# Kernel tuning notes

Hardware: AMD Instinct MI355X
Metric: run time of the kernel (lower is better)

## Reference

```python
import jax, jax.numpy as jnp
import numpy as np
from jax import lax

SLOPE = 0.01  # nn.LeakyReLU default negative slope

def leaky(x):
    return jnp.where(x >= 0, x, SLOPE * x)

def conv2d(x, w, b, pad):
    # x: [N,C,H,W], w: [O,I,kh,kw]
    y = lax.conv_general_dilated(x, w, (1, 1), [(pad, pad), (pad, pad)],
                                 dimension_numbers=('NCHW', 'OIHW', 'NCHW'))
    return y + b[None, :, None, None]

def centered_ifftn(x, axes):
    # np.fft.fftshift(np.fft.ifftn(np.fft.ifftshift(X), norm='ortho'))
    return jnp.fft.fftshift(jnp.fft.ifftn(jnp.fft.ifftshift(x, axes=axes), axes=axes, norm='ortho'), axes=axes)

def setup_inputs() -> dict:
    key = jax.random.key(0)
    ks = jax.random.split(key, 10)
    B, H, W, CK = 8, 640, 368, 32
    return {
        'img':    jax.random.normal(ks[0], (B, 1, H, W), jnp.float32),
        'kspace': jax.random.normal(ks[1], (B, 2, H, W), jnp.float32),
        # k_model1: Conv2d(2, CK, 3, padding=1) + LeakyReLU
        'wk': jax.random.normal(ks[2], (CK, 2, 3, 3), jnp.float32) * 0.1,
        'bk': jnp.zeros((CK,), jnp.float32),
        # conv1: Conv2d(CK, 2, kernel_size=1)
        'w1': jax.random.normal(ks[3], (2, CK, 1, 1), jnp.float32) * 0.1,
        'b1': jnp.zeros((2,), jnp.float32),
        # conv2: Conv2d(2, 1, kernel_size=1)
        'w2': jax.random.normal(ks[4], (1, 2, 1, 1), jnp.float32) * 0.1,
        'b2': jnp.zeros((1,), jnp.float32),
        # i_model1: Conv2d(1, 1, 3, padding=1) + LeakyReLU
        'wi': jax.random.normal(ks[5], (1, 1, 3, 3), jnp.float32) * 0.1,
        'bi': jnp.zeros((1,), jnp.float32),
    }

def reference(img, kspace, wk, bk, w1, b1, w2, b2, wi, bi):
    # k-space branch: k_model1 then conv1 + LeakyReLU
    out1 = leaky(conv2d(leaky(conv2d(kspace, wk, bk, 1)), w1, b1, 0))  # [B,2,H,W]
    # channel 0 = real, channel 1 = imag; ifftn over ALL axes (incl. batch),
    # exactly as the original numpy call with axes=range(out.ndim)
    cplx = out1[:, 0].astype(jnp.complex64) + 1j * out1[:, 1].astype(jnp.complex64)  # [B,H,W]
    im = jnp.abs(centered_ifftn(cplx, (0, 1, 2)))[:, None]  # [B,1,H,W]
    # concat with image, cast to half (torch.cuda.HalfTensor), conv2 + LeakyReLU
    out = jnp.concatenate([im, img], axis=1).astype(jnp.float16)  # [B,2,H,W]
    out = leaky(conv2d(out, w2.astype(jnp.float16), b2.astype(jnp.float16), 0))
    out = out.astype(jnp.float32)  # [B,1,H,W]
    # image-domain model
    return leaky(conv2d(out, wi, bi, 1))  # [B,1,H,W]
```

## Files before the change

### kernel.cpp

```cpp
#include <hip/hip_runtime.h>
#include <hip/hip_fp16.h>
#include <math.h>

#define B_ 8
#define H_ 640
#define W_ 368
#define HW_ (H_*W_)
#define NP_ (B_*H_*W_)

#define WLINES 8
#define HLINES 4
#define HP 645
#define TS 16

typedef __attribute__((ext_vector_type(8))) short v8s;
typedef __attribute__((ext_vector_type(4))) float v4f;

__device__ __forceinline__ float leaky_(float x){ return fmaxf(x, 0.01f*x); }

__device__ __forceinline__ unsigned short f2bf(float x){
    unsigned u = __float_as_uint(x);
    u += 0x7FFFu + ((u >> 16) & 1u);
    return (unsigned short)(u >> 16);
}

__device__ __forceinline__ float2 cadd_(float2 a, float2 b){ return make_float2(a.x+b.x, a.y+b.y); }
__device__ __forceinline__ float2 csub_(float2 a, float2 b){ return make_float2(a.x-b.x, a.y-b.y); }
__device__ __forceinline__ float2 cmul_(float2 a, float c, float s){
    return make_float2(a.x*c - a.y*s, a.x*s + a.y*c);
}
__device__ __forceinline__ float2 cmulv_(float2 a, float2 w){
    return make_float2(a.x*w.x - a.y*w.y, a.x*w.y + a.y*w.x);
}

__device__ __forceinline__ void dft4p_(float2 p0, float2 p1, float2 p2, float2 p3,
                                       float2& z0, float2& z1, float2& z2, float2& z3){
    float2 s0 = cadd_(p0,p2), d0 = csub_(p0,p2);
    float2 s1 = cadd_(p1,p3), d1 = csub_(p1,p3);
    z0 = cadd_(s0,s1);
    z2 = csub_(s0,s1);
    z1 = make_float2(d0.x - d1.y, d0.y + d1.x);
    z3 = make_float2(d0.x + d1.y, d0.y - d1.x);
}

__device__ __forceinline__ void fft16p_(const float2* x, float2* X){
    const float C1 = 0.9238795325112867f, S1 = 0.3826834323650898f;
    const float R  = 0.7071067811865476f;
    float2 Y[4][4];
    #pragma unroll
    for (int b = 0; b < 4; ++b)
        dft4p_(x[b], x[4+b], x[8+b], x[12+b], Y[b][0], Y[b][1], Y[b][2], Y[b][3]);
    Y[1][1] = cmul_(Y[1][1],  C1,  S1);
    Y[1][2] = cmul_(Y[1][2],   R,   R);
    Y[1][3] = cmul_(Y[1][3],  S1,  C1);
    Y[2][1] = cmul_(Y[2][1],   R,   R);
    Y[2][2] = make_float2(-Y[2][2].y, Y[2][2].x);
    Y[2][3] = cmul_(Y[2][3],  -R,   R);
    Y[3][1] = cmul_(Y[3][1],  S1,  C1);
    Y[3][2] = cmul_(Y[3][2],  -R,   R);
    Y[3][3] = cmul_(Y[3][3], -C1, -S1);
    #pragma unroll
    for (int c = 0; c < 4; ++c)
        dft4p_(Y[0][c], Y[1][c], Y[2][c], Y[3][c], X[c], X[c+4], X[c+8], X[c+12]);
}

__device__ __forceinline__ void fft8p_(const float2* x, float2* X){
    const float R = 0.7071067811865476f;
    float2 Y0[4], Y1[4];
    dft4p_(x[0], x[2], x[4], x[6], Y0[0], Y0[1], Y0[2], Y0[3]);
    dft4p_(x[1], x[3], x[5], x[7], Y1[0], Y1[1], Y1[2], Y1[3]);
    float2 T0 = Y1[0];
    float2 T1 = cmul_(Y1[1],  R, R);
    float2 T2 = make_float2(-Y1[2].y, Y1[2].x);
    float2 T3 = cmul_(Y1[3], -R, R);
    X[0] = cadd_(Y0[0], T0);  X[4] = csub_(Y0[0], T0);
    X[1] = cadd_(Y0[1], T1);  X[5] = csub_(Y0[1], T1);
    X[2] = cadd_(Y0[2], T2);  X[6] = csub_(Y0[2], T2);
    X[3] = cadd_(Y0[3], T3);  X[7] = csub_(Y0[3], T3);
}

__global__ void init_tables_kernel(float2* __restrict__ T){
    int i = blockIdx.x*blockDim.x + threadIdx.x;
    if (i >= 1301) return;
    int r, c, modN; int j;
    if      (i <  368){ j = i;        r = j%16; c = j/16; modN = 368; }
    else if (i < 1008){ j = i-368;    r = j%16; c = j/16; modN = 640; }
    else if (i < 1048){ j = i-1008;   r = j%8;  c = j/8;  modN = 40;  }
    else              { j = i-1048;   r = j/11; c = j%11 + 1; modN = 23; }
    int t = (int)(((long long)r * c) % modN);
    if (t > modN/2) t -= modN;
    float ang = (float)(6.283185307179586 * ((double)t / (double)modN));
    float s, co;
    sincosf(ang, &s, &co);
    T[i] = make_float2(co, s);
}

__global__ __launch_bounds__(256) void kbranch_mfma(const float* __restrict__ ksp,
                               const float* __restrict__ wk,
                               const float* __restrict__ bk,
                               const float* __restrict__ w1,
                               const float* __restrict__ b1,
                               float2* __restrict__ A){
    __shared__ unsigned short Sb[2616];
    __shared__ unsigned short Wr[4*512];
    int t = threadIdx.x;
    int bh = blockIdx.x;
    int h = bh % 640, b = bh / 640;

    for (int i = t; i < 2616; i += 256){
        float val = 0.f;
        if (i < 2232){
            int rr = i / 372, col = i - rr*372;
            int r = rr >> 1, ic = rr & 1;
            int hh = h - 1 + r, sc = col - 1;
            if ((unsigned)hh < 640u && (unsigned)sc < 368u)
                val = ksp[((b*2 + ic)*640 + hh)*368 + sc];
        }
        Sb[i] = f2bf(val);
    }

    int lane = t & 63, wave = t >> 6;
    int oc = lane & 15, q = lane >> 4;
    int off[8];
    v8s bf0, bf1, b2f;
    #pragma unroll
    for (int j = 0; j < 8; ++j){
        int kk = q*8 + j;
        if (kk < 18){
            int ic = (kk >= 9) ? 1 : 0;
            int tt = kk - ic*9;
            int ty = tt/3, tx = tt - ty*3;
            off[j] = (ty*2 + ic)*372 + tx;
            bf0[j] = (short)f2bf(wk[oc*18 + kk]);
            bf1[j] = (short)f2bf(wk[(oc+16)*18 + kk]);
        } else {
            off[j] = 2232;
            bf0[j] = 0; bf1[j] = 0;
        }
        b2f[j] = (oc < 2) ? (short)f2bf(w1[oc*32 + kk]) : (short)0;
    }
    float bk0 = bk[oc], bk1 = bk[oc+16];
    float biasn = (oc == 1) ? b1[1] : b1[0];
    unsigned short* Wrw = Wr + (wave << 9);
    __syncthreads();

    int gbase = wave*6;
    int cnt = (wave < 3) ? 6 : 5;
    for (int i = 0; i < cnt; ++i){
        int g = gbase + i;
        int w0m = g*16 + oc;
        v8s af;
        #pragma unroll
        for (int j = 0; j < 8; ++j) af[j] = (short)Sb[off[j] + w0m];
        v4f d0 = {0.f,0.f,0.f,0.f}, d1 = {0.f,0.f,0.f,0.f};
        d0 = __builtin_amdgcn_mfma_f32_16x16x32_bf16(af, bf0, d0, 0, 0, 0);
        d1 = __builtin_amdgcn_mfma_f32_16x16x32_bf16(af, bf1, d1, 0, 0, 0);
        #pragma unroll
        for (int r = 0; r < 4; ++r){
            int px = q*4 + r;
            Wrw[px*32 + oc]      = f2bf(leaky_(d0[r] + bk0));
            Wrw[px*32 + 16 + oc] = f2bf(leaky_(d1[r] + bk1));
        }
        asm volatile("s_waitcnt lgkmcnt(0)" ::: "memory");
        const v8s* ap = (const v8s*)(Wrw + oc*32);
        v8s a2 = ap[q];
        v4f d2 = {0.f,0.f,0.f,0.f};
        d2 = __builtin_amdgcn_mfma_f32_16x16x32_bf16(a2, b2f, d2, 0, 0, 0);
        float vals[4], ov[4];
        #pragma unroll
        for (int r = 0; r < 4; ++r){
            vals[r] = leaky_(biasn + d2[r]);
            ov[r] = __shfl_xor(vals[r], 1);
        }
        if (oc == 0){
            float2* dst = A + (size_t)bh*368 + g*16 + q*4;
            *(float4*)dst       = make_float4(vals[0], ov[0], vals[1], ov[1]);
            *(float4*)(dst + 2) = make_float4(vals[2], ov[2], vals[3], ov[3]);
        }
        asm volatile("s_waitcnt lgkmcnt(0)" ::: "memory");
    }
}

__global__ __launch_bounds__(256) void fftW_kernel(const float2* __restrict__ A,
                                                   const float2* __restrict__ TW368P,
                                                   const float2* __restrict__ F23P,
                                                   float2* __restrict__ Bt){
    __shared__ float2 X[WLINES*369];
    int t = threadIdx.x;
    size_t base = (size_t)blockIdx.x * (WLINES*368);

    for (int i = t; i < WLINES*368; i += 256){
        int l = i / 368, n = i - l*368;
        float2 v = A[base + i];
        float s = (n & 1) ? -1.f : 1.f;
        X[l*369 + n] = make_float2(v.x*s, v.y*s);
    }
    __syncthreads();

    if (t < 184){
        int l = t & 7, n2 = t >> 3;
        float2 xr[16], Xo[16];
        #pragma unroll
        for (int n1 = 0; n1 < 16; ++n1) xr[n1] = X[l*369 + 23*n1 + n2];
        fft16p_(xr, Xo);
        const float2* row = TW368P + n2*16;
        #pragma unroll
        for (int k1 = 0; k1 < 16; ++k1)
            X[l*369 + 23*k1 + n2] = cmulv_(Xo[k1], row[k1]);
    }
    __syncthreads();

    {
        int l = t & 7, k1 = (t >> 3) & 15, half = t >> 7;
        const float2* xp = X + l*369 + 23*k1;
        float2 x0 = xp[0];
        float2 u[11], d[11];
        #pragma unroll
        for (int m = 1; m <= 11; ++m){
            float2 a = xp[m], bb = xp[23-m];
            u[m-1] = cadd_(a, bb);
            d[m-1] = csub_(a, bb);
        }
        __syncthreads();
        int k2beg = half ? 12 : 0;
        int k2end = half ? 23 : 12;
        for (int k2 = k2beg; k2 < k2end; ++k2){
            const float2* row = F23P + k2*11;
            float re = x0.x, im = x0.y;
            #pragma unroll
            for (int m = 0; m < 11; ++m){
                float c = row[m].x, s = row[m].y;
                re += u[m].x*c - d[m].y*s;
                im += u[m].y*c + d[m].x*s;
            }
            X[l*369 + k1 + 16*k2] = make_float2(re, im);
        }
    }
    __syncthreads();

    const float sc = 0.052129458158616354f;
    int b  = blockIdx.x / 80;
    int h0 = (blockIdx.x - b*80) * WLINES;
    for (int i = t; i < WLINES*368; i += 256){
        int k = i >> 3, l = i & 7;
        float2 v = X[l*369 + k];
        float s = (k & 1) ? -sc : sc;
        Bt[((size_t)(b*368 + k))*640 + h0 + l] = make_float2(v.x*s, v.y*s);
    }
}

__global__ __launch_bounds__(256) void fftH_kernel(const float2* __restrict__ Bt,
                                                   const float2* __restrict__ TW640P,
                                                   const float2* __restrict__ TW40P,
                                                   float2* __restrict__ A2){
    __shared__ float2 X[HLINES*HP];
    int t = threadIdx.x;
    size_t base = (size_t)blockIdx.x * (HLINES*640);

    for (int i = t; i < HLINES*640; i += 256){
        int l = i / 640, n = i - l*640;
        float2 v = Bt[base + i];
        float s = (n & 1) ? -1.f : 1.f;
        X[l*HP + n] = make_float2(v.x*s, v.y*s);
    }
    __syncthreads();

    if (t < 160){
        int l = t & 3, n2 = t >> 2;
        float2 xr[16], Xo[16];
        #pragma unroll
        for (int n1 = 0; n1 < 16; ++n1) xr[n1] = X[l*HP + 40*n1 + n2];
        fft16p_(xr, Xo);
        const float2* row = TW640P + n2*16;
        #pragma unroll
        for (int k1 = 0; k1 < 16; ++k1)
            X[l*HP + 40*k1 + n2] = cmulv_(Xo[k1], row[k1]);
    }
    __syncthreads();

    for (int it = t; it < 320; it += 256){
        int l = it & 3, k1 = (it >> 2) & 15, m2 = it >> 6;
        float2 xr[8], Xo[8];
        #pragma unroll
        for (int m1 = 0; m1 < 8; ++m1) xr[m1] = X[l*HP + 40*k1 + 5*m1 + m2];
        fft8p_(xr, Xo);
        const float2* row = TW40P + m2*8;
        #pragma unroll
        for (int j1 = 0; j1 < 8; ++j1)
            X[l*HP + 40*k1 + 5*j1 + m2] = cmulv_(Xo[j1], row[j1]);
    }
    __syncthreads();

    {
        const float CK1[5] = {1.f,  0.30901699437494745f, -0.8090169943749475f, -0.8090169943749475f,  0.30901699437494745f};
        const float SK1[5] = {0.f,  0.9510565162951535f,   0.5877852522924731f, -0.5877852522924731f, -0.9510565162951535f};
        const float CK2[5] = {1.f, -0.8090169943749475f,   0.30901699437494745f, 0.30901699437494745f, -0.8090169943749475f};
        const float SK2[5] = {0.f,  0.5877852522924731f,  -0.9510565162951535f,  0.9510565162951535f, -0.5877852522924731f};
        int it0 = t, it1 = t + 256;
        int l0 = it0 & 3, k10 = (it0 >> 2) & 15, j10 = it0 >> 6;
        int l1 = it1 & 3, k11 = (it1 >> 2) & 15, j11 = it1 >> 6;
        float2 p0[5], p1[5];
        #pragma unroll
        for (int m2 = 0; m2 < 5; ++m2) p0[m2] = X[l0*HP + 40*k10 + 5*j10 + m2];
        #pragma unroll
        for (int m2 = 0; m2 < 5; ++m2) p1[m2] = X[l1*HP + 40*k11 + 5*j11 + m2];
        __syncthreads();
        float2 u0a = cadd_(p0[1], p0[4]), d0a = csub_(p0[1], p0[4]);
        float2 u0b = cadd_(p0[2], p0[3]), d0b = csub_(p0[2], p0[3]);
        float2 u1a = cadd_(p1[1], p1[4]), d1a = csub_(p1[1], p1[4]);
        float2 u1b = cadd_(p1[2], p1[3]), d1b = csub_(p1[2], p1[3]);
        #pragma unroll
        for (int j2 = 0; j2 < 5; ++j2){
            float c1v = CK1[j2], s1v = SK1[j2], c2v = CK2[j2], s2v = SK2[j2];
            float re0 = p0[0].x + u0a.x*c1v - d0a.y*s1v + u0b.x*c2v - d0b.y*s2v;
            float im0 = p0[0].y + u0a.y*c1v + d0a.x*s1v + u0b.y*c2v + d0b.x*s2v;
            float re1 = p1[0].x + u1a.x*c1v - d1a.y*s1v + u1b.x*c2v - d1b.y*s2v;
            float im1 = p1[0].y + u1a.y*c1v + d1a.x*s1v + u1b.y*c2v + d1b.x*s2v;
            X[l0*HP + k10 + 16*j10 + 128*j2] = make_float2(re0, im0);
            X[l1*HP + k11 + 16*j11 + 128*j2] = make_float2(re1, im1);
        }
    }
    __syncthreads();

    const float sc = 0.03952847075210474f;
    for (int i = t; i < HLINES*640; i += 256){
        int l = i / 640, k = i - l*640;
        float2 v = X[l*HP + k];
        float s = (k & 1) ? -sc : sc;
        A2[base + i] = make_float2(v.x*s, v.y*s);
    }
}

__global__ __launch_bounds__(256) void tail_kernel(const float2* __restrict__ A2,
                                  const float* __restrict__ img,
                                  const float* __restrict__ w2,
                                  const float* __restrict__ b2,
                                  const float* __restrict__ wi,
                                  const float* __restrict__ bi,
                                  float* __restrict__ out){
    __shared__ float Pl[8][TS+2][TS+3];
    int t = threadIdx.x;
    int ty0 = (blockIdx.x / 23) * TS;
    int tx0 = (blockIdx.x % 23) * TS;

    float w2h0 = __half2float(__float2half(w2[0]));
    float w2h1 = __half2float(__float2half(w2[1]));
    float b2h  = __half2float(__float2half(b2[0]));
    const float sc8 = 0.35355339059327373f;

    for (int idx = t; idx < (TS+2)*(TS+2); idx += 256){
        int hx = idx / (TS+2), hy = idx - hx*(TS+2);
        int hh = ty0 - 1 + hy, ww = tx0 - 1 + hx;
        int hc = min(max(hh, 0), H_-1), wc = min(max(ww, 0), W_-1);
        float2 x[8], Xo[8];
        #pragma unroll
        for (int n = 0; n < 8; ++n){
            float2 v = A2[((size_t)(n*368 + wc))*640 + hc];
            float s = (n & 1) ? -1.f : 1.f;
            x[n] = make_float2(v.x*s, v.y*s);
        }
        fft8p_(x, Xo);
        #pragma unroll
        for (int k = 0; k < 8; ++k){
            float s = (k & 1) ? -sc8 : sc8;
            float yr = Xo[k].x * s, yi = Xo[k].y * s;
            float mag = sqrtf(yr*yr + yi*yi);
            Pl[k][hy][hx] = __half2float(__float2half(mag));
        }
    }
    __syncthreads();

    for (int idx = t; idx < (TS+2)*(TS+2); idx += 256){
        int hy = idx / (TS+2), hx = idx - hy*(TS+2);
        int hh = ty0 - 1 + hy, ww = tx0 - 1 + hx;
        bool inb = (hh >= 0) && (hh < H_) && (ww >= 0) && (ww < W_);
        int hc = min(max(hh, 0), H_-1), wc = min(max(ww, 0), W_-1);
        float inbf = inb ? 1.f : 0.f;
        #pragma unroll
        for (int k = 0; k < 8; ++k){
            float g = __half2float(__float2half(img[(size_t)k*HW_ + hc*W_ + wc]));
            float a = Pl[k][hy][hx];
            float o = leaky_(a*w2h0 + g*w2h1 + b2h);
            o = __half2float(__float2half(o));
            Pl[k][hy][hx] = o * inbf;
        }
    }
    __syncthreads();

    int sy = t >> 4, sx = t & 15;
    float wv[9];
    #pragma unroll
    for (int q = 0; q < 9; ++q) wv[q] = wi[q];
    float bi0 = bi[0];
    #pragma unroll
    for (int k = 0; k < 8; ++k){
        float acc = bi0;
        #pragma unroll
        for (int dy = 0; dy < 3; ++dy)
            #pragma unroll
            for (int dx = 0; dx < 3; ++dx)
                acc += wv[dy*3+dx] * Pl[k][sy+dy][sx+dx];
        out[((size_t)k*H_ + ty0+sy)*W_ + tx0+sx] = leaky_(acc);
    }
}

extern "C" void kernel_launch(void* const* d_in, const int* in_sizes, int n_in,
                              void* d_out, int out_size, void* d_ws, size_t ws_size,
                              hipStream_t stream){
    const float* img = (const float*)d_in[0];
    const float* ksp = (const float*)d_in[1];
    const float* wk  = (const float*)d_in[2];
    const float* bk  = (const float*)d_in[3];
    const float* w1  = (const float*)d_in[4];
    const float* b1  = (const float*)d_in[5];
    const float* w2  = (const float*)d_in[6];
    const float* b2  = (const float*)d_in[7];
    const float* wi  = (const float*)d_in[8];
    const float* bi  = (const float*)d_in[9];

    char* ws = (char*)d_ws;
    float2* A   = (float2*)(ws + 0);
    float2* Bt  = (float2*)(ws + 15073280);
    float2* T   = (float2*)(ws + 30146560);
    float2* TW368P = T + 0;
    float2* TW640P = T + 368;
    float2* TW40P  = T + 1008;
    float2* F23P   = T + 1048;
    float* out  = (float*)d_out;

    init_tables_kernel<<<6, 256, 0, stream>>>(T);

    kbranch_mfma<<<B_*H_, 256, 0, stream>>>(ksp, wk, bk, w1, b1, A);

    fftW_kernel<<<(B_*H_)/WLINES, 256, 0, stream>>>(A, TW368P, F23P, Bt);
    fftH_kernel<<<(B_*W_)/HLINES, 256, 0, stream>>>(Bt, TW640P, TW40P, A);

    tail_kernel<<<(H_/TS)*(W_/TS), 256, 0, stream>>>(A, img, w2, b2, wi, bi, out);
}
```

Measured before the change: 172.8 us.

## Fuse k-space conv branch with W-direction FFT in one kernel

Merges the MFMA convolution kernel and the W-axis FFT kernel so each block computes the conv output for 4 rows directly into shared memory and then runs the row FFT there. This removes the global write and re-read of the intermediate complex array A and one kernel launch. In exchange each block handles fewer FFT lines (4 instead of 8), uses more shared memory, and the FFT stages leave more threads idle.

```diff
diff --git a/kernel.cpp b/kernel.cpp
--- a/kernel.cpp
+++ b/kernel.cpp
@@ -8,7 +8,7 @@
 #define HW_ (H_*W_)
 #define NP_ (B_*H_*W_)
 
-#define WLINES 8
+#define FROWS 4
 #define HLINES 4
 #define HP 645
 #define TS 16
@@ -95,32 +95,39 @@
     T[i] = make_float2(co, s);
 }
 
-__global__ __launch_bounds__(256) void kbranch_mfma(const float* __restrict__ ksp,
+__global__ __launch_bounds__(256) void kfftw_kernel(const float* __restrict__ ksp,
                                const float* __restrict__ wk,
                                const float* __restrict__ bk,
                                const float* __restrict__ w1,
                                const float* __restrict__ b1,
-                               float2* __restrict__ A){
-    __shared__ unsigned short Sb[2616];
+                               const float2* __restrict__ TW368P,
+                               const float2* __restrict__ F23P,
+                               float2* __restrict__ Bt){
+    __shared__ unsigned short Sb[4836];
     __shared__ unsigned short Wr[4*512];
+    __shared__ float2 X[FROWS*369];
     int t = threadIdx.x;
-    int bh = blockIdx.x;
-    int h = bh % 640, b = bh / 640;
-
-    for (int i = t; i < 2616; i += 256){
-        float val = 0.f;
-        if (i < 2232){
-            int rr = i / 372, col = i - rr*372;
-            int r = rr >> 1, ic = rr & 1;
-            int hh = h - 1 + r, sc = col - 1;
-            if ((unsigned)hh < 640u && (unsigned)sc < 368u)
-                val = ksp[((b*2 + ic)*640 + hh)*368 + sc];
-        }
-        Sb[i] = f2bf(val);
-    }
+    int blk = blockIdx.x;
+    int b  = blk / 160;
+    int h0 = (blk - b*160) * FROWS;
+
+    for (int seg = 0; seg < 12; ++seg){
+        int r = seg >> 1, ic = seg & 1;
+        int hh = h0 - 1 + r;
+        int ok = ((unsigned)hh < 640u);
+        const float* base = ksp + ((size_t)(b*2 + ic)*640 + (ok ? hh : 0))*368;
+        for (int col = t; col < 372; col += 256){
+            int c = col - 1;
+            float v = (ok && (unsigned)c < 368u) ? base[c] : 0.f;
+            Sb[seg*372 + col] = f2bf(v);
+        }
+    }
+    for (int i = t; i < 372; i += 256) Sb[4464 + i] = 0;
 
     int lane = t & 63, wave = t >> 6;
     int oc = lane & 15, q = lane >> 4;
+    int l = wave;
+
     int off[8];
     v8s bf0, bf1, b2f;
     #pragma unroll
@@ -130,11 +137,11 @@
             int ic = (kk >= 9) ? 1 : 0;
             int tt = kk - ic*9;
             int ty = tt/3, tx = tt - ty*3;
-            off[j] = (ty*2 + ic)*372 + tx;
+            off[j] = ((ty + l)*2 + ic)*372 + tx;
             bf0[j] = (short)f2bf(wk[oc*18 + kk]);
             bf1[j] = (short)f2bf(wk[(oc+16)*18 + kk]);
         } else {
-            off[j] = 2232;
+            off[j] = 4464;
             bf0[j] = 0; bf1[j] = 0;
         }
         b2f[j] = (oc < 2) ? (short)f2bf(w1[oc*32 + kk]) : (short)0;
@@ -144,10 +151,7 @@
     unsigned short* Wrw = Wr + (wave << 9);
     __syncthreads();
 
-    int gbase = wave*6;
-    int cnt = (wave < 3) ? 6 : 5;
-    for (int i = 0; i < cnt; ++i){
-        int g = gbase + i;
+    for (int g = 0; g < 23; ++g){
         int w0m = g*16 + oc;
         v8s af;
         #pragma unroll
@@ -173,46 +177,32 @@
             ov[r] = __shfl_xor(vals[r], 1);
         }
         if (oc == 0){
-            float2* dst = A + (size_t)bh*368 + g*16 + q*4;
-            *(float4*)dst       = make_float4(vals[0], ov[0], vals[1], ov[1]);
-            *(float4*)(dst + 2) = make_float4(vals[2], ov[2], vals[3], ov[3]);
+            int px = g*16 + q*4;
+            X[l*369 + px  ] = make_float2( vals[0],  ov[0]);
+            X[l*369 + px+1] = make_float2(-vals[1], -ov[1]);
+            X[l*369 + px+2] = make_float2( vals[2],  ov[2]);
+            X[l*369 + px+3] = make_float2(-vals[3], -ov[3]);
         }
         asm volatile("s_waitcnt lgkmcnt(0)" ::: "memory");
     }
-}
-
-__global__ __launch_bounds__(256) void fftW_kernel(const float2* __restrict__ A,
-                                                   const float2* __restrict__ TW368P,
-                                                   const float2* __restrict__ F23P,
-                                                   float2* __restrict__ Bt){
-    __shared__ float2 X[WLINES*369];
-    int t = threadIdx.x;
-    size_t base = (size_t)blockIdx.x * (WLINES*368);
-
-    for (int i = t; i < WLINES*368; i += 256){
-        int l = i / 368, n = i - l*368;
-        float2 v = A[base + i];
-        float s = (n & 1) ? -1.f : 1.f;
-        X[l*369 + n] = make_float2(v.x*s, v.y*s);
-    }
-    __syncthreads();
-
-    if (t < 184){
-        int l = t & 7, n2 = t >> 3;
+    __syncthreads();
+
+    if (t < 92){
+        int ll = t & 3, n2 = t >> 2;
         float2 xr[16], Xo[16];
         #pragma unroll
-        for (int n1 = 0; n1 < 16; ++n1) xr[n1] = X[l*369 + 23*n1 + n2];
+        for (int n1 = 0; n1 < 16; ++n1) xr[n1] = X[ll*369 + 23*n1 + n2];
         fft16p_(xr, Xo);
         const float2* row = TW368P + n2*16;
         #pragma unroll
         for (int k1 = 0; k1 < 16; ++k1)
-            X[l*369 + 23*k1 + n2] = cmulv_(Xo[k1], row[k1]);
+            X[ll*369 + 23*k1 + n2] = cmulv_(Xo[k1], row[k1]);
     }
     __syncthreads();
 
     {
-        int l = t & 7, k1 = (t >> 3) & 15, half = t >> 7;
-        const float2* xp = X + l*369 + 23*k1;
+        int ll = t & 3, k1 = (t >> 2) & 15, qr = t >> 6;
+        const float2* xp = X + ll*369 + 23*k1;
         float2 x0 = xp[0];
         float2 u[11], d[11];
         #pragma unroll
@@ -222,8 +212,8 @@
             d[m-1] = csub_(a, bb);
         }
         __syncthreads();
-        int k2beg = half ? 12 : 0;
-        int k2end = half ? 23 : 12;
+        int k2beg = qr*6;
+        int k2end = (qr == 3) ? 23 : k2beg + 6;
         for (int k2 = k2beg; k2 < k2end; ++k2){
             const float2* row = F23P + k2*11;
             float re = x0.x, im = x0.y;
@@ -233,19 +223,17 @@
                 re += u[m].x*c - d[m].y*s;
                 im += u[m].y*c + d[m].x*s;
             }
-            X[l*369 + k1 + 16*k2] = make_float2(re, im);
+            X[ll*369 + k1 + 16*k2] = make_float2(re, im);
         }
     }
     __syncthreads();
 
     const float sc = 0.052129458158616354f;
-    int b  = blockIdx.x / 80;
-    int h0 = (blockIdx.x - b*80) * WLINES;
-    for (int i = t; i < WLINES*368; i += 256){
-        int k = i >> 3, l = i & 7;
-        float2 v = X[l*369 + k];
+    for (int i = t; i < FROWS*368; i += 256){
+        int k = i >> 2, ll = i & 3;
+        float2 v = X[ll*369 + k];
         float s = (k & 1) ? -sc : sc;
-        Bt[((size_t)(b*368 + k))*640 + h0 + l] = make_float2(v.x*s, v.y*s);
+        Bt[((size_t)(b*368 + k))*640 + h0 + ll] = make_float2(v.x*s, v.y*s);
     }
 }
 
@@ -419,8 +407,8 @@
     const float* bi  = (const float*)d_in[9];
 
     char* ws = (char*)d_ws;
-    float2* A   = (float2*)(ws + 0);
-    float2* Bt  = (float2*)(ws + 15073280);
+    float2* Bt  = (float2*)(ws + 0);
+    float2* A2  = (float2*)(ws + 15073280);
     float2* T   = (float2*)(ws + 30146560);
     float2* TW368P = T + 0;
     float2* TW640P = T + 368;
@@ -430,10 +418,8 @@
 
     init_tables_kernel<<<6, 256, 0, stream>>>(T);
 
-    kbranch_mfma<<<B_*H_, 256, 0, stream>>>(ksp, wk, bk, w1, b1, A);
-
-    fftW_kernel<<<(B_*H_)/WLINES, 256, 0, stream>>>(A, TW368P, F23P, Bt);
-    fftH_kernel<<<(B_*W_)/HLINES, 256, 0, stream>>>(Bt, TW640P, TW40P, A);
-
-    tail_kernel<<<(H_/TS)*(W_/TS), 256, 0, stream>>>(A, img, w2, b2, wi, bi, out);
-}
+    kfftw_kernel<<<B_*(H_/FROWS), 256, 0, stream>>>(ksp, wk, bk, w1, b1,
+                                                    TW368P, F23P, Bt);
+    fftH_kernel<<<(B_*W_)/HLINES, 256, 0, stream>>>(Bt, TW640P, TW40P, A2);
+    tail_kernel<<<(H_/TS)*(W_/TS), 256, 0, stream>>>(A2, img, w2, b2, wi, bi, out);
+}
```

Result: no change. 172.4 us (-0.2%).
